# Kernel optimization log

Measured on AMD Instinct MI355X. Metric: run time of the kernel, lower is better.

The kernel has to match this reference:

```python
import jax, jax.numpy as jnp
import numpy as np

N_NODES = 100000
N_EDGES = 1600000
IN_DIM = 29
OUT_DIM = 64
BN_EPS = 1e-5


def setup_inputs() -> dict:
    key = jax.random.key(0)
    k1, k2, k3, k4, k5, k6, k7, k8 = jax.random.split(key, 8)
    node = jax.random.normal(k1, (N_NODES, 3), dtype=jnp.float32)
    features = jax.random.normal(k2, (N_NODES, IN_DIM), dtype=jnp.float32)
    edges = jax.random.randint(k3, (N_EDGES, 2), 0, N_NODES, dtype=jnp.int64)
    # Linear(input_dim+3, output_dim, bias=False): weight [out, in+3]
    fan_in = IN_DIM + 3
    weight = jax.random.uniform(k4, (OUT_DIM, fan_in), dtype=jnp.float32,
                                minval=-1.0, maxval=1.0) / np.sqrt(fan_in)
    # BatchNorm1d(output_dim) in eval mode: affine params + running stats
    gamma = jax.random.normal(k5, (OUT_DIM,), dtype=jnp.float32) * 0.1 + 1.0
    beta = jax.random.normal(k6, (OUT_DIM,), dtype=jnp.float32) * 0.1
    running_mean = jax.random.normal(k7, (OUT_DIM,), dtype=jnp.float32) * 0.1
    running_var = jax.random.uniform(k8, (OUT_DIM,), dtype=jnp.float32,
                                     minval=0.5, maxval=1.5)
    return {"node": node, "features": features, "edges": edges,
            "weight": weight, "gamma": gamma, "beta": beta,
            "running_mean": running_mean, "running_var": running_var}


def reference(node, features, edges, weight, gamma, beta, running_mean, running_var):
    dst = edges[:, 0]  # pos_i index (pooling destination)
    src = edges[:, 1]  # pos_j / x_j index
    # gather + concat: msg [E, in+3]
    msg = jnp.concatenate([features[src], node[src] - node[dst]], axis=1)
    # Linear (no bias): [E, out]
    msg = jnp.einsum('ei,oi->eo', msg, weight)
    # BatchNorm1d (eval mode, running stats)
    inv_std = gamma / jnp.sqrt(running_var + BN_EPS)
    msg = (msg - running_mean) * inv_std + beta
    # scatter-max pooling over destination nodes (fixed N segments;
    # torch.unique + scatter_reduce(amax) == segment_max restricted to covered
    # nodes; empty segments filled with 0 matching the zeros init)
    pooled = jax.ops.segment_max(msg, dst, num_segments=N_NODES)
    return jnp.where(jnp.isneginf(pooled), 0.0, pooled)
```

## Files before the change

kernel.cpp:

```cpp
#include <hip/hip_runtime.h>
#include <hip/hip_fp16.h>

#define IN_DIM 29
#define XDIM 32
#define OUT_DIM 64
#define BN_EPS 1e-5f

#define BW      32
#define BW_LOG  5
#define TNODES  64
#define MAXBUCK 4096
#define SENT    0


__global__ __launch_bounds__(256) void fused_tc_kernel(
    const float* __restrict__ features, const float* __restrict__ node,
    const float* __restrict__ weight, const float* __restrict__ gamma,
    const float* __restrict__ rvar, unsigned short* __restrict__ yq,
    const int* __restrict__ edges, int* __restrict__ gHist,
    int n_nodes, int n_edges, int nbuck, int chunk, int nblk)
{
    __shared__ __align__(16) int smem[MAXBUCK];
    if ((int)blockIdx.x < nblk) {
        int* h = smem;
        for (int i = threadIdx.x; i < nbuck; i += 256) h[i] = 0;
        __syncthreads();
        const int e0 = blockIdx.x * chunk;
        const int e1 = min(e0 + chunk, n_edges);
        const int np = (e1 - e0) >> 1;
        const int4* ep4 = (const int4*)(edges + 2 * e0);
        for (int p = threadIdx.x; p < np; p += 256) {
            int4 v = ep4[p];
            atomicAdd(&h[v.x >> BW_LOG], 1);
            atomicAdd(&h[v.z >> BW_LOG], 1);
        }
        if (((e1 - e0) & 1) && threadIdx.x == 0)
            atomicAdd(&h[edges[2 * (e1 - 1)] >> BW_LOG], 1);
        __syncthreads();
        for (int i = threadIdx.x; i < nbuck; i += 256)
            gHist[i * nblk + blockIdx.x] = h[i];
    } else {
        float* stage = (float*)smem;
        const int tid  = threadIdx.x;
        const int lane = tid & 63, wid = tid >> 6;
        const int n0   = ((int)blockIdx.x - nblk) * TNODES;
        const int nrem = min(TNODES, n_nodes - n0);

        for (int idx = tid; idx < nrem * XDIM; idx += 256) {
            const int r = idx >> 5, c = idx & 31;
            float v = (c < IN_DIM) ? features[(size_t)(n0 + r) * IN_DIM + c]
                                   : node[(size_t)(n0 + r) * 3 + (c - IN_DIM)];
            stage[idx] = v;
        }

        const float a = gamma[lane] * __frsqrt_rn(rvar[lane] + BN_EPS);
        float w[XDIM];
        const float4* wp = (const float4*)(weight + lane * XDIM);
#pragma unroll
        for (int q = 0; q < 8; ++q) {
            float4 v = wp[q];
            w[4*q+0] = v.x * a; w[4*q+1] = v.y * a;
            w[4*q+2] = v.z * a; w[4*q+3] = v.w * a;
        }
        __syncthreads();

        const int r0 = wid * (TNODES / 4);
        const int r1 = min(r0 + TNODES / 4, nrem);
        for (int r = r0; r < r1; ++r) {
            const float4* xs = (const float4*)(stage + r * XDIM);
            float a0 = 0.f, a1 = 0.f, a2 = 0.f, a3 = 0.f;
#pragma unroll
            for (int q = 0; q < 8; ++q) {
                float4 x = xs[q];
                a0 = fmaf(x.x, w[4*q+0], a0);
                a1 = fmaf(x.y, w[4*q+1], a1);
                a2 = fmaf(x.z, w[4*q+2], a2);
                a3 = fmaf(x.w, w[4*q+3], a3);
            }
            const float acc = (a0 + a1) + (a2 + a3);
            unsigned short hh = __half_as_ushort(__float2half(acc));
            unsigned short enc = (hh & 0x8000) ? (unsigned short)(~hh)
                                               : (unsigned short)(hh | 0x8000);
            yq[(size_t)(n0 + r) * OUT_DIM + lane] = enc;
        }
    }
}

__global__ __launch_bounds__(256) void scan_a_kernel(
    int* __restrict__ data, int n, int* __restrict__ aux)
{
    const int t = threadIdx.x;
    const int base = blockIdx.x * 1024 + t * 4;
    int v[4];
#pragma unroll
    for (int k = 0; k < 4; ++k) v[k] = (base + k < n) ? data[base + k] : 0;
    int tsum = v[0] + v[1] + v[2] + v[3];

    const int lane = t & 63, wv = t >> 6;
    int x = tsum;
#pragma unroll
    for (int off = 1; off < 64; off <<= 1) {
        int y = __shfl_up(x, off);
        if (lane >= off) x += y;
    }
    __shared__ int wsum[4];
    if (lane == 63) wsum[wv] = x;
    __syncthreads();
    int wexcl = 0;
    for (int i = 0; i < wv; ++i) wexcl += wsum[i];
    int run = wexcl + x - tsum;
#pragma unroll
    for (int k = 0; k < 4; ++k) {
        if (base + k < n) data[base + k] = run;
        run += v[k];
    }
    if (t == 255) aux[blockIdx.x] = run;
}

__global__ __launch_bounds__(256) void scan_b_kernel(int* __restrict__ aux, int nb) {
    const int t = threadIdx.x;
    const int lane = t & 63, wv = t >> 6;
    __shared__ int wsum[4];
    __shared__ int s_run;
    if (t == 0) s_run = 0;
    __syncthreads();
    for (int base = 0; base < nb; base += 256) {
        const int i = base + t;
        int v = (i < nb) ? aux[i] : 0;
        int x = v;
#pragma unroll
        for (int off = 1; off < 64; off <<= 1) {
            int y = __shfl_up(x, off);
            if (lane >= off) x += y;
        }
        if (lane == 63) wsum[wv] = x;
        __syncthreads();
        int wexcl = 0;
        for (int k = 0; k < wv; ++k) wexcl += wsum[k];
        const int run = s_run;
        if (i < nb) aux[i] = run + wexcl + x - v;
        __syncthreads();
        if (t == 255) s_run = run + wexcl + x;
        __syncthreads();
    }
}

__global__ __launch_bounds__(512) void partition_kernel(
    const int* __restrict__ edges, const int* __restrict__ gOffs,
    const int* __restrict__ aux,
    int* __restrict__ keys, int n_edges, int nbuck, int chunk, int nblk)
{
    __shared__ int cur[MAXBUCK];
    for (int i = threadIdx.x; i < nbuck; i += 512) {
        const int idx = i * nblk + blockIdx.x;
        cur[i] = gOffs[idx] + aux[idx >> 10];
    }
    __syncthreads();
    const int e0 = blockIdx.x * chunk;
    const int e1 = min(e0 + chunk, n_edges);
    const int np = (e1 - e0) >> 1;
    const int4* ep4 = (const int4*)(edges + 2 * e0);
    for (int p = threadIdx.x; p < np; p += 512) {
        int4 v = ep4[p];
        const int b0 = v.x >> BW_LOG;
        const int p0 = atomicAdd(&cur[b0], 1);
        keys[p0] = (v.x & (BW - 1)) | (v.y << BW_LOG);
        const int b1 = v.z >> BW_LOG;
        const int p1 = atomicAdd(&cur[b1], 1);
        keys[p1] = (v.z & (BW - 1)) | (v.w << BW_LOG);
    }
    if (((e1 - e0) & 1) && threadIdx.x == 0) {
        const int dst = edges[2 * (e1 - 1)], src = edges[2 * (e1 - 1) + 1];
        const int b = dst >> BW_LOG;
        const int pos = atomicAdd(&cur[b], 1);
        keys[pos] = (dst & (BW - 1)) | (src << BW_LOG);
    }
}

__global__ __launch_bounds__(512) void pool_fused_kernel(
    const int* __restrict__ gOffs, const int* __restrict__ aux,
    const int* __restrict__ keys,
    const unsigned short* __restrict__ yq, const float* __restrict__ node,
    const float* __restrict__ weight, const float* __restrict__ gamma,
    const float* __restrict__ beta, const float* __restrict__ rmean,
    const float* __restrict__ rvar,
    float* __restrict__ out, int n_nodes, int n_edges, int nbuck, int nblk)
{
    __shared__ int acc[BW * OUT_DIM];
    const int tid = threadIdx.x;
    const int lane = tid & 63, wid = tid >> 6;
    const int b = blockIdx.x;

    {
        int4* p = (int4*)acc;
        for (int i = tid; i < BW * OUT_DIM / 4; i += 512)
            p[i] = make_int4(SENT, SENT, SENT, SENT);
    }
    __syncthreads();

    const int i0 = b * nblk;
    const int beg = gOffs[i0] + aux[i0 >> 10];
    int end;
    if (b == nbuck - 1) end = n_edges;
    else {
        const int i1 = (b + 1) * nblk;
        end = gOffs[i1] + aux[i1 >> 10];
    }

    const int cnt = end - beg;
    const int slice = (cnt + 7) >> 3;
    const int w_beg = beg + wid * slice;
    const int w_end = min(w_beg + slice, end);

    if (w_beg < w_end) {
        const int last = w_end - 1;
        int j = w_beg;
        int kv = keys[min(j + lane, last)];
        while (j < w_end) {
            const int jn = j + 64;
            int kv_n = 0;
            if (jn < w_end) kv_n = keys[min(jn + lane, last)];

#pragma unroll
            for (int g = 0; g < 8; ++g) {
                unsigned int va[8]; int da[8];
#pragma unroll
                for (int u = 0; u < 8; ++u) {
                    const int key = __builtin_amdgcn_readlane(kv, g * 8 + u);
                    da[u] = key & (BW - 1);
                    va[u] = yq[(size_t)((unsigned)key >> BW_LOG) * OUT_DIM + lane];
                }
#pragma unroll
                for (int u = 0; u < 8; ++u)
                    atomicMax(&acc[da[u] * OUT_DIM + lane], (int)va[u]);
            }
            j = jn; kv = kv_n;
        }
    }
    __syncthreads();

    const float a  = gamma[lane] * __frsqrt_rn(rvar[lane] + BN_EPS);
    const float bp = beta[lane] - rmean[lane] * a;
    const float w29 = weight[lane * XDIM + 29] * a;
    const float w30 = weight[lane * XDIM + 30] * a;
    const float w31 = weight[lane * XDIM + 31] * a;

    for (int d = wid; d < BW; d += 8) {
        const int dg = b * BW + d;
        if (dg >= n_nodes) break;
        const int k = acc[d * OUT_DIM + lane];
        float rr;
        if (k == SENT) {
            rr = 0.0f;
        } else {
            const unsigned short enc = (unsigned short)k;
            const unsigned short h = (enc & 0x8000) ? (unsigned short)(enc ^ 0x8000)
                                                    : (unsigned short)(~enc);
            const float v = __half2float(__ushort_as_half(h));
            const float nx = node[(size_t)dg * 3 + 0];
            const float ny = node[(size_t)dg * 3 + 1];
            const float nz = node[(size_t)dg * 3 + 2];
            rr = v + (bp - (w29 * nx + w30 * ny + w31 * nz));
        }
        out[(size_t)dg * OUT_DIM + lane] = rr;
    }
}

__global__ void init_kernel(int4* __restrict__ out, int total4) {
    int t = blockIdx.x * blockDim.x + threadIdx.x;
    if (t < total4) out[t] = make_int4(INT_MIN, INT_MIN, INT_MIN, INT_MIN);
}

__global__ __launch_bounds__(256) void edge_atomic_kernel(
    const int* __restrict__ edges,
    const float* __restrict__ features, const float* __restrict__ node,
    const float* __restrict__ weight, const float* __restrict__ gamma,
    const float* __restrict__ beta, const float* __restrict__ rmean,
    const float* __restrict__ rvar,
    int* __restrict__ out, int n_edges, int epw)
{
    const int lane = threadIdx.x & 63;
    const int wave = (blockIdx.x * blockDim.x + threadIdx.x) >> 6;
    int e0 = wave * epw, e1 = e0 + epw;
    if (e1 > n_edges) e1 = n_edges;

    float w[XDIM];
    const float4* wp = (const float4*)(weight + lane * XDIM);
#pragma unroll
    for (int q = 0; q < 8; ++q) {
        float4 v = wp[q];
        w[4*q+0] = v.x; w[4*q+1] = v.y; w[4*q+2] = v.z; w[4*q+3] = v.w;
    }
    const float a = gamma[lane] * __frsqrt_rn(rvar[lane] + BN_EPS);
    const float bprime = beta[lane] - rmean[lane] * a;

    for (int e = e0; e < e1; ++e) {
        const int dst = edges[2*e+0], src = edges[2*e+1];
        float x[XDIM];
#pragma unroll
        for (int i = 0; i < IN_DIM; ++i) x[i] = features[(size_t)src * IN_DIM + i];
#pragma unroll
        for (int j = 0; j < 3; ++j)
            x[IN_DIM+j] = node[(size_t)src*3+j] - node[(size_t)dst*3+j];
        float acc = 0.0f;
#pragma unroll
        for (int i = 0; i < XDIM; ++i) acc = fmaf(x[i], w[i], acc);
        float msg = fmaf(acc, a, bprime);
        int bb = __float_as_int(msg);
        int key = (bb < 0) ? (bb ^ 0x7FFFFFFF) : bb;
        atomicMax(out + (size_t)dst * OUT_DIM + lane, key);
    }
}

__global__ void decode_kernel(int* __restrict__ out, int total) {
    int t = blockIdx.x * blockDim.x + threadIdx.x;
    if (t >= total) return;
    int k = out[t];
    float r;
    if (k == INT_MIN) r = 0.0f;
    else { int b = (k < 0) ? (k ^ 0x7FFFFFFF) : k; r = __int_as_float(b); }
    ((float*)out)[t] = r;
}

extern "C" void kernel_launch(void* const* d_in, const int* in_sizes, int n_in,
                              void* d_out, int out_size, void* d_ws, size_t ws_size,
                              hipStream_t stream) {
    const float* node     = (const float*)d_in[0];
    const float* features = (const float*)d_in[1];
    const int*   edges    = (const int*)d_in[2];
    const float* weight   = (const float*)d_in[3];
    const float* gamma    = (const float*)d_in[4];
    const float* beta     = (const float*)d_in[5];
    const float* rmean    = (const float*)d_in[6];
    const float* rvar     = (const float*)d_in[7];

    const int n_nodes = in_sizes[0] / 3;
    const int n_edges = in_sizes[2] / 2;

    const int nbuck = (n_nodes + BW - 1) >> BW_LOG;

    int nblk = 0; size_t o_yq=0, o_hist=0, o_aux=0, o_keys=0; size_t need = 0;
    for (int cand = 256; cand >= 32; cand >>= 1) {
        const int n_scan = nbuck * cand;
        const int nb_scan = (n_scan + 1023) / 1024;
        size_t off = 0;
        auto alloc = [&](size_t bytes) { size_t r = off; off = (off + bytes + 15) & ~(size_t)15; return r; };
        o_yq   = alloc((size_t)n_nodes * OUT_DIM * sizeof(unsigned short));
        o_hist = alloc((size_t)n_scan * sizeof(int));
        o_aux  = alloc((size_t)nb_scan * sizeof(int));
        o_keys = alloc((size_t)n_edges * sizeof(int));
        need = off;
        if (need <= ws_size) { nblk = cand; break; }
    }

    if (nblk > 0 && nbuck <= MAXBUCK && n_nodes <= MAXBUCK * BW) {
        const int n_scan = nbuck * nblk;
        const int nb_scan = (n_scan + 1023) / 1024;
        int chunk = (n_edges + nblk - 1) / nblk;
        chunk = (chunk + 1) & ~1;
        const int ntb = (n_nodes + TNODES - 1) / TNODES;

        char* base  = (char*)d_ws;
        unsigned short* yq = (unsigned short*)(base + o_yq);
        int* gHist  = (int*)(base + o_hist);
        int* aux    = (int*)(base + o_aux);
        int* keys   = (int*)(base + o_keys);

        fused_tc_kernel<<<nblk + ntb, 256, 0, stream>>>(
            features, node, weight, gamma, rvar, yq,
            edges, gHist, n_nodes, n_edges, nbuck, chunk, nblk);
        scan_a_kernel<<<nb_scan, 256, 0, stream>>>(gHist, n_scan, aux);
        scan_b_kernel<<<1, 256, 0, stream>>>(aux, nb_scan);
        partition_kernel<<<nblk, 512, 0, stream>>>(edges, gHist, aux, keys,
                                                   n_edges, nbuck, chunk, nblk);
        pool_fused_kernel<<<nbuck, 512, 0, stream>>>(
            gHist, aux, keys, yq, node, weight, gamma, beta, rmean, rvar,
            (float*)d_out, n_nodes, n_edges, nbuck, nblk);
    } else {
        int* out_i = (int*)d_out;
        const int total4 = out_size / 4;
        init_kernel<<<(total4 + 255) / 256, 256, 0, stream>>>((int4*)out_i, total4);
        const int n_waves = 8192;
        const int epw = (n_edges + n_waves - 1) / n_waves;
        edge_atomic_kernel<<<n_waves / 4, 256, 0, stream>>>(
            edges, features, node, weight, gamma, beta, rmean, rvar,
            out_i, n_edges, epw);
        decode_kernel<<<(out_size + 255) / 256, 256, 0, stream>>>(out_i, out_size);
    }
}
```

Measured before the change: 187.6 us.

## Sort bucket keys by destination in shared memory and reduce per-wave in registers

The pooling kernel now counting-sorts each bucket's edge keys by local destination into shared memory (histogram, wave-level prefix scan, scatter). Each wave then computes the max for its four destination nodes in registers with batched gathers, replacing per-edge LDS atomicMax into a 32x64 accumulator. Large buckets fall back to the old atomic path. Launch bounds now request 4 blocks per CU. The sort adds extra passes over the keys and several barriers, and load balance now depends on per-destination degree.

Result: slower. 191.5 us (+2.1%).

```diff
diff --git a/kernel.cpp b/kernel.cpp
--- a/kernel.cpp
+++ b/kernel.cpp
@@ -10,6 +10,7 @@
 #define BW_LOG  5
 #define TNODES  64
 #define MAXBUCK 4096
+#define KCAP    4096
 #define SENT    0
 
 
@@ -177,7 +178,7 @@
     }
 }
 
-__global__ __launch_bounds__(512) void pool_fused_kernel(
+__global__ __launch_bounds__(512, 4) void pool_fused_kernel(
     const int* __restrict__ gOffs, const int* __restrict__ aux,
     const int* __restrict__ keys,
     const unsigned short* __restrict__ yq, const float* __restrict__ node,
@@ -186,17 +187,11 @@
     const float* __restrict__ rvar,
     float* __restrict__ out, int n_nodes, int n_edges, int nbuck, int nblk)
 {
-    __shared__ int acc[BW * OUT_DIM];
+    __shared__ int skeys[KCAP];
+    __shared__ int hcnt[BW], hoff[BW + 1], hcur[BW];
     const int tid = threadIdx.x;
     const int lane = tid & 63, wid = tid >> 6;
     const int b = blockIdx.x;
-
-    {
-        int4* p = (int4*)acc;
-        for (int i = tid; i < BW * OUT_DIM / 4; i += 512)
-            p[i] = make_int4(SENT, SENT, SENT, SENT);
-    }
-    __syncthreads();
 
     const int i0 = b * nblk;
     const int beg = gOffs[i0] + aux[i0 >> 10];
@@ -206,38 +201,7 @@
         const int i1 = (b + 1) * nblk;
         end = gOffs[i1] + aux[i1 >> 10];
     }
-
     const int cnt = end - beg;
-    const int slice = (cnt + 7) >> 3;
-    const int w_beg = beg + wid * slice;
-    const int w_end = min(w_beg + slice, end);
-
-    if (w_beg < w_end) {
-        const int last = w_end - 1;
-        int j = w_beg;
-        int kv = keys[min(j + lane, last)];
-        while (j < w_end) {
-            const int jn = j + 64;
-            int kv_n = 0;
-            if (jn < w_end) kv_n = keys[min(jn + lane, last)];
-
-#pragma unroll
-            for (int g = 0; g < 8; ++g) {
-                unsigned int va[8]; int da[8];
-#pragma unroll
-                for (int u = 0; u < 8; ++u) {
-                    const int key = __builtin_amdgcn_readlane(kv, g * 8 + u);
-                    da[u] = key & (BW - 1);
-                    va[u] = yq[(size_t)((unsigned)key >> BW_LOG) * OUT_DIM + lane];
-                }
-#pragma unroll
-                for (int u = 0; u < 8; ++u)
-                    atomicMax(&acc[da[u] * OUT_DIM + lane], (int)va[u]);
-            }
-            j = jn; kv = kv_n;
-        }
-    }
-    __syncthreads();
 
     const float a  = gamma[lane] * __frsqrt_rn(rvar[lane] + BN_EPS);
     const float bp = beta[lane] - rmean[lane] * a;
@@ -245,24 +209,104 @@
     const float w30 = weight[lane * XDIM + 30] * a;
     const float w31 = weight[lane * XDIM + 31] * a;
 
-    for (int d = wid; d < BW; d += 8) {
-        const int dg = b * BW + d;
-        if (dg >= n_nodes) break;
-        const int k = acc[d * OUT_DIM + lane];
-        float rr;
-        if (k == SENT) {
-            rr = 0.0f;
-        } else {
-            const unsigned short enc = (unsigned short)k;
-            const unsigned short h = (enc & 0x8000) ? (unsigned short)(enc ^ 0x8000)
-                                                    : (unsigned short)(~enc);
-            const float v = __half2float(__ushort_as_half(h));
-            const float nx = node[(size_t)dg * 3 + 0];
-            const float ny = node[(size_t)dg * 3 + 1];
-            const float nz = node[(size_t)dg * 3 + 2];
-            rr = v + (bp - (w29 * nx + w30 * ny + w31 * nz));
-        }
-        out[(size_t)dg * OUT_DIM + lane] = rr;
+    if (cnt <= KCAP) {
+        if (tid < BW) hcnt[tid] = 0;
+        __syncthreads();
+        for (int i = tid; i < cnt; i += 512)
+            atomicAdd(&hcnt[keys[beg + i] & (BW - 1)], 1);
+        __syncthreads();
+        if (tid < 64) {
+            int v = (lane < BW) ? hcnt[lane] : 0;
+            int x = v;
+#pragma unroll
+            for (int off = 1; off < BW; off <<= 1) {
+                int y = __shfl_up(x, off);
+                if (lane >= off) x += y;
+            }
+            if (lane < BW) { hoff[lane] = x - v; hcur[lane] = x - v; }
+            if (lane == BW - 1) hoff[BW] = x;
+        }
+        __syncthreads();
+        for (int i = tid; i < cnt; i += 512) {
+            const int key = keys[beg + i];
+            const int p = atomicAdd(&hcur[key & (BW - 1)], 1);
+            skeys[p] = key;
+        }
+        __syncthreads();
+
+#pragma unroll
+        for (int q = 0; q < 4; ++q) {
+            const int d = wid + (q << 3);
+            const int k0 = hoff[d], k1 = hoff[d + 1];
+            unsigned int m = SENT;
+            int kk = k0;
+            for (; kk + 8 <= k1; kk += 8) {
+                unsigned int src[8];
+#pragma unroll
+                for (int u = 0; u < 8; ++u)
+                    src[u] = ((unsigned)skeys[kk + u]) >> BW_LOG;
+                unsigned int vv[8];
+#pragma unroll
+                for (int u = 0; u < 8; ++u)
+                    vv[u] = yq[(size_t)src[u] * OUT_DIM + lane];
+                __builtin_amdgcn_sched_barrier(0);
+#pragma unroll
+                for (int u = 0; u < 8; ++u)
+                    m = m > vv[u] ? m : vv[u];
+            }
+            for (; kk < k1; ++kk) {
+                const unsigned int s = ((unsigned)skeys[kk]) >> BW_LOG;
+                const unsigned int v = yq[(size_t)s * OUT_DIM + lane];
+                m = m > v ? m : v;
+            }
+            const int dg = b * BW + d;
+            if (dg < n_nodes) {
+                float rr;
+                if (m == SENT) {
+                    rr = 0.0f;
+                } else {
+                    const unsigned short enc = (unsigned short)m;
+                    const unsigned short h = (enc & 0x8000) ? (unsigned short)(enc ^ 0x8000)
+                                                            : (unsigned short)(~enc);
+                    const float v = __half2float(__ushort_as_half(h));
+                    const float nx = node[(size_t)dg * 3 + 0];
+                    const float ny = node[(size_t)dg * 3 + 1];
+                    const float nz = node[(size_t)dg * 3 + 2];
+                    rr = v + (bp - (w29 * nx + w30 * ny + w31 * nz));
+                }
+                out[(size_t)dg * OUT_DIM + lane] = rr;
+            }
+        }
+    } else {
+        int* acc = skeys;
+        for (int i = tid; i < BW * OUT_DIM; i += 512) acc[i] = SENT;
+        __syncthreads();
+        for (int i = beg + wid; i < end; i += 8) {
+            const int key = keys[i];
+            const int d = key & (BW - 1);
+            const unsigned int v = yq[(size_t)((unsigned)key >> BW_LOG) * OUT_DIM + lane];
+            atomicMax(&acc[d * OUT_DIM + lane], (int)v);
+        }
+        __syncthreads();
+        for (int d = wid; d < BW; d += 8) {
+            const int dg = b * BW + d;
+            if (dg >= n_nodes) break;
+            const int k = acc[d * OUT_DIM + lane];
+            float rr;
+            if (k == SENT) {
+                rr = 0.0f;
+            } else {
+                const unsigned short enc = (unsigned short)k;
+                const unsigned short h = (enc & 0x8000) ? (unsigned short)(enc ^ 0x8000)
+                                                        : (unsigned short)(~enc);
+                const float v = __half2float(__ushort_as_half(h));
+                const float nx = node[(size_t)dg * 3 + 0];
+                const float ny = node[(size_t)dg * 3 + 1];
+                const float nz = node[(size_t)dg * 3 + 2];
+                rr = v + (bp - (w29 * nx + w30 * ny + w31 * nz));
+            }
+            out[(size_t)dg * OUT_DIM + lane] = rr;
+        }
     }
 }
 
```
